# Optimization experiments

Hardware: AMD Instinct MI355X
Metric: run time of the kernel (lower is better)

The kernel has to match this reference:

```python
import jax, jax.numpy as jnp
import numpy as np

B, N, K, D, F, H = 8, 512, 16, 256, 1024, 8


def _ln(x, g, b):
    m = jnp.mean(x, axis=-1, keepdims=True)
    v = jnp.var(x, axis=-1, keepdims=True)
    return (x - m) / jnp.sqrt(v + 1e-5) * g + b


def _mlp(x, W1, b1, W2, b2):
    return jax.nn.gelu(x @ W1 + b1, approximate=False) @ W2 + b2


def setup_inputs() -> dict:
    key = jax.random.key(0)
    ks = jax.random.split(key, 16)
    s = 0.02
    inp = {
        'x': jax.random.normal(ks[0], (N, B, D), jnp.float32),
        'e': jax.random.normal(ks[1], (B, N, K, D), jnp.float32),
        'edge_index': jax.random.randint(ks[2], (B, N, K), 0, N),
        'Wq': jax.random.normal(ks[3], (D, D), jnp.float32) * s,
        'bq': jnp.zeros((D,), jnp.float32),
        'Wk': jax.random.normal(ks[4], (D, D), jnp.float32) * s,
        'bk': jnp.zeros((D,), jnp.float32),
        'Wv': jax.random.normal(ks[5], (D, D), jnp.float32) * s,
        'bv': jnp.zeros((D,), jnp.float32),
        'Wo': jax.random.normal(ks[6], (D, D), jnp.float32) * s,
        'bo': jnp.zeros((D,), jnp.float32),
        'nW1': jax.random.normal(ks[7], (D, F), jnp.float32) * s,
        'nb1': jnp.zeros((F,), jnp.float32),
        'nW2': jax.random.normal(ks[8], (F, D), jnp.float32) * s,
        'nb2': jnp.zeros((D,), jnp.float32),
        'eW1': jax.random.normal(ks[9], (D, F), jnp.float32) * s,
        'eb1': jnp.zeros((F,), jnp.float32),
        'eW2': jax.random.normal(ks[10], (F, D), jnp.float32) * s,
        'eb2': jnp.zeros((D,), jnp.float32),
        'na_g': jnp.ones((D,), jnp.float32), 'na_b': jnp.zeros((D,), jnp.float32),
        'ea_g': jnp.ones((D,), jnp.float32), 'ea_b': jnp.zeros((D,), jnp.float32),
        'nf_g': jnp.ones((D,), jnp.float32), 'nf_b': jnp.zeros((D,), jnp.float32),
        'ef_g': jnp.ones((D,), jnp.float32), 'ef_b': jnp.zeros((D,), jnp.float32),
    }
    return inp


def reference(x, e, edge_index, Wq, bq, Wk, bk, Wv, bv, Wo, bo,
              nW1, nb1, nW2, nb2, eW1, eb1, eW2, eb2,
              na_g, na_b, ea_g, ea_b, nf_g, nf_b, ef_g, ef_b):
    n, b, d = x.shape
    hd = d // H
    xt = jnp.transpose(x, (1, 0, 2))  # (B, N, D) residual in batch-first layout
    bi = jnp.arange(b)[:, None, None]
    ni = jnp.arange(n)[None, :, None]

    # scatter edge features into dense additive attention bias (B, N, N)
    attn_bias = jnp.zeros((b, n, n), x.dtype).at[bi, ni, edge_index].set(e.mean(-1))

    def heads(t):  # (B,N,D) -> (B,H,N,hd)
        return t.reshape(b, n, H, hd).transpose(0, 2, 1, 3)

    q = heads(xt @ Wq + bq) * (hd ** -0.5)
    k = heads(xt @ Wk + bk)
    v = heads(xt @ Wv + bv)
    logits = jnp.einsum('bhnd,bhmd->bhnm', q, k) + attn_bias[:, None]
    attn = jax.nn.softmax(logits, axis=-1)  # (B,H,N,N)
    out = jnp.einsum('bhnm,bhmd->bhnd', attn, v)
    out = out.transpose(0, 2, 1, 3).reshape(b, n, d) @ Wo + bo

    xn = _ln(xt + out, na_g, na_b)  # (B,N,D)

    # edge update: gather attn weights and neighbor node features via edge_index
    weights = attn.mean(axis=1)  # (B,N,N) head-averaged
    w = weights[bi, edge_index, ni]  # (B,N,K): weights[b, edge_index[b,n,k], n]
    gathered = xt[jnp.arange(b)[:, None, None], edge_index]  # (B,N,K,D)
    e2 = _ln(e + w[..., None] * gathered, ea_g, ea_b)

    xn = _ln(xn + _mlp(xn, nW1, nb1, nW2, nb2), nf_g, nf_b)
    e2 = _ln(e2 + _mlp(e2, eW1, eb1, eW2, eb2), ef_g, ef_b)
    return jnp.transpose(xn, (1, 0, 2)), e2
```

## Files before the change

### kernel.cpp

```cpp
#include <hip/hip_runtime.h>
#include <hip/hip_bf16.h>
#include <math.h>

#define B_ 8
#define N_ 512
#define K_ 16
#define D_ 256
#define F_ 1024
#define H_ 8
#define HD_ 32
#define M_ (B_*N_)
#define R_ (B_*N_*K_)

typedef __bf16 bf16x8 __attribute__((ext_vector_type(8)));
typedef float  f32x4  __attribute__((ext_vector_type(4)));

__device__ inline short bf16s(float f) {
    __hip_bfloat16 h = __float2bfloat16(f);
    return *reinterpret_cast<short*>(&h);
}
__device__ inline float b2f(short s) {
    union { float f; unsigned u; } v; v.u = ((unsigned)(unsigned short)s) << 16; return v.f;
}

__device__ __forceinline__ void gload16(const short* g, short* l) {
    __builtin_amdgcn_global_load_lds(
        (const __attribute__((address_space(1))) unsigned int*)g,
        (__attribute__((address_space(3))) unsigned int*)l, 16, 0, 0);
}

__global__ __launch_bounds__(256) void transposeAll(
        const float* __restrict__ Wq, const float* __restrict__ Wk,
        const float* __restrict__ Wv, const float* __restrict__ Wo,
        const float* __restrict__ nW1, const float* __restrict__ nW2,
        const float* __restrict__ eW1, const float* __restrict__ eW2,
        short* __restrict__ WqkvT, short* __restrict__ WoT,
        short* __restrict__ nW1T, short* __restrict__ nW2T,
        short* __restrict__ eW1T, short* __restrict__ eW2T)
{
    const float* W; short* WT; int Kk, Nn; float sc = 1.f;
    switch (blockIdx.z) {
        case 0: W=Wq;  WT=WqkvT;          Kk=256;  Nn=256;  sc=0.17677669529663687f; break;
        case 1: W=Wk;  WT=WqkvT+256*256;  Kk=256;  Nn=256;  break;
        case 2: W=Wv;  WT=WqkvT+512*256;  Kk=256;  Nn=256;  break;
        case 3: W=Wo;  WT=WoT;            Kk=256;  Nn=256;  break;
        case 4: W=nW1; WT=nW1T;           Kk=256;  Nn=1024; break;
        case 5: W=nW2; WT=nW2T;           Kk=1024; Nn=256;  break;
        case 6: W=eW1; WT=eW1T;           Kk=256;  Nn=1024; break;
        default:W=eW2; WT=eW2T;           Kk=1024; Nn=256;  break;
    }
    const int bx = blockIdx.x, by = blockIdx.y;
    if (bx >= Nn/32 || by >= Kk/32) return;
    __shared__ float tile[32][33];
    int tx = threadIdx.x & 31, ty = threadIdx.x >> 5;
    #pragma unroll
    for (int j = 0; j < 4; ++j) {
        int k = by*32 + ty + j*8;
        tile[ty + j*8][tx] = W[(size_t)k*Nn + bx*32 + tx];
    }
    __syncthreads();
    #pragma unroll
    for (int j = 0; j < 4; ++j) {
        int n = bx*32 + ty + j*8;
        WT[(size_t)n*Kk + by*32 + tx] = bf16s(tile[tx][ty + j*8] * sc);
    }
}

__global__ __launch_bounds__(256) void build_bqkv(const float* __restrict__ bq,
        const float* __restrict__ bk, const float* __restrict__ bv,
        float* __restrict__ bqkv)
{
    int t = blockIdx.x*256 + threadIdx.x;
    if (t >= 768) return;
    float v = (t < 256) ? bq[t]*0.17677669529663687f
            : (t < 512) ? bk[t-256] : bv[t-512];
    bqkv[t] = v;
}

__global__ __launch_bounds__(256) void conv_x(const float* __restrict__ x,
        short* __restrict__ xtb)
{
    int row = blockIdx.x;
    int d = threadIdx.x;
    int b = row >> 9, n = row & 511;
    xtb[(size_t)row*D_ + d] = bf16s(x[((size_t)n*B_ + b)*D_ + d]);
}

__global__ __launch_bounds__(256) void edge_means(const float* __restrict__ e,
        float* __restrict__ means)
{
    long row = (long)blockIdx.x*4 + (threadIdx.x >> 6);
    int lane = threadIdx.x & 63;
    float4 v = ((const float4*)(e + row*D_))[lane];
    float s = v.x + v.y + v.z + v.w;
    for (int o = 1; o < 64; o <<= 1) s += __shfl_xor(s, o);
    if (lane == 0) means[row] = s * (1.f/D_);
}

__global__ __launch_bounds__(256) void bias_build(const int* __restrict__ ei,
        const float* __restrict__ means, float* __restrict__ biasb)
{
    const int r0 = blockIdx.x * 16;
    float4* bp4 = (float4*)(biasb + (size_t)r0*N_);
    #pragma unroll
    for (int i = threadIdx.x; i < 16*N_/4; i += 256)
        bp4[i] = make_float4(0.f, 0.f, 0.f, 0.f);
    __syncthreads();
    if (threadIdx.x < 16) {
        const int idx = r0 + threadIdx.x;
        const int* ep = ei + (size_t)idx*K_;
        const float* mp = means + (size_t)idx*K_;
        float* bp = biasb + (size_t)idx*N_;
        for (int k = 0; k < K_; ++k) bp[ep[k]] = mp[k];
    }
}

template<int OUTMODE>
__global__ __launch_bounds__(256) void gemm_bf16(
        const short* __restrict__ A, const short* __restrict__ BT,
        const float* __restrict__ bias, float* __restrict__ Cf,
        short* __restrict__ Cb, short* __restrict__ vtb, int Nn, int Kk)
{
    __shared__ __align__(16) short As[128*32];
    __shared__ __align__(16) short Bs[128*32];
    const int t = threadIdx.x;
    const int lane = t & 63;
    const int wave = t >> 6;
    const int wr = (wave >> 1) * 64;
    const int wc = (wave & 1) * 64;
    const int bm = blockIdx.x, bn = blockIdx.y;
    f32x4 acc[4][4] = {};
    const int srow = lane >> 2;
    const int sk   = (lane & 3) * 8;
    const int fr = lane & 15;
    const int fk = (lane >> 4) * 8;
    for (int k0 = 0; k0 < Kk; k0 += 32) {
        __syncthreads();
        #pragma unroll
        for (int i = 0; i < 2; ++i) {
            const int rb = wave*16 + i*64;
            gload16(A  + (size_t)(bm*128 + rb + srow)*Kk + k0 + sk, &As[rb*32]);
            gload16(BT + (size_t)(bn*128 + rb + srow)*Kk + k0 + sk, &Bs[rb*32]);
        }
        __syncthreads();
        bf16x8 af[4], bfr[4];
        #pragma unroll
        for (int i2 = 0; i2 < 4; ++i2)
            af[i2] = *(const bf16x8*)&As[(wr + i2*16 + fr)*32 + fk];
        #pragma unroll
        for (int n2 = 0; n2 < 4; ++n2)
            bfr[n2] = *(const bf16x8*)&Bs[(wc + n2*16 + fr)*32 + fk];
        #pragma unroll
        for (int i2 = 0; i2 < 4; ++i2)
            #pragma unroll
            for (int n2 = 0; n2 < 4; ++n2)
                acc[i2][n2] = __builtin_amdgcn_mfma_f32_16x16x32_bf16(
                        af[i2], bfr[n2], acc[i2][n2], 0, 0, 0);
    }
    const int fq4 = (lane >> 4) * 4;
    #pragma unroll
    for (int i2 = 0; i2 < 4; ++i2) {
        #pragma unroll
        for (int n2 = 0; n2 < 4; ++n2) {
            const int col = bn*128 + wc + n2*16 + fr;
            const float bv = bias[col];
            if constexpr (OUTMODE == 2) {
                const int rowb = bm*128 + wr + i2*16 + fq4;
                if (col < 512) {
                    #pragma unroll
                    for (int r2 = 0; r2 < 4; ++r2)
                        Cb[(size_t)(rowb + r2)*512 + col] = bf16s(acc[i2][n2][r2] + bv);
                } else {
                    const int b = rowb >> 9, n = rowb & 511;
                    const int dv = col - 512, h = dv >> 5, dh = dv & 31;
                    short4 s4;
                    s4.x = bf16s(acc[i2][n2][0] + bv);
                    s4.y = bf16s(acc[i2][n2][1] + bv);
                    s4.z = bf16s(acc[i2][n2][2] + bv);
                    s4.w = bf16s(acc[i2][n2][3] + bv);
                    *(short4*)&vtb[((size_t)((b*H_ + h)*HD_ + dh))*512 + n] = s4;
                }
            } else {
                #pragma unroll
                for (int r2 = 0; r2 < 4; ++r2) {
                    const int row = bm*128 + wr + i2*16 + fq4 + r2;
                    Cf[(size_t)row*Nn + col] = acc[i2][n2][r2] + bv;
                }
            }
        }
    }
}

__global__ __launch_bounds__(512, 4) void gemm_gelu(
        const short* __restrict__ A, const short* __restrict__ BT,
        const float* __restrict__ bias, short* __restrict__ Cb, int Nn, int Kk)
{
    __shared__ __align__(16) short As[128*32];
    __shared__ __align__(16) short Bs[256*32];
    const int t = threadIdx.x;
    const int lane = t & 63;
    const int wave = t >> 6;
    const int wrg = (wave >> 2) * 64;
    const int wc  = (wave & 3) * 64;
    const int bm = blockIdx.x, bn = blockIdx.y;
    f32x4 acc[4][4] = {};
    const int srow = lane >> 2;
    const int sk   = (lane & 3) * 8;
    const int fr = lane & 15;
    const int fk = (lane >> 4) * 8;
    for (int k0 = 0; k0 < Kk; k0 += 32) {
        __syncthreads();
        {
            const int rb = wave*16;
            gload16(A + (size_t)(bm*128 + rb + srow)*Kk + k0 + sk, &As[rb*32]);
        }
        #pragma unroll
        for (int i = 0; i < 2; ++i) {
            const int rb = wave*16 + i*128;
            gload16(BT + (size_t)(bn*256 + rb + srow)*Kk + k0 + sk, &Bs[rb*32]);
        }
        __syncthreads();
        bf16x8 af[4], bfr[4];
        #pragma unroll
        for (int i2 = 0; i2 < 4; ++i2)
            af[i2] = *(const bf16x8*)&As[(wrg + i2*16 + fr)*32 + fk];
        #pragma unroll
        for (int n2 = 0; n2 < 4; ++n2)
            bfr[n2] = *(const bf16x8*)&Bs[(wc + n2*16 + fr)*32 + fk];
        #pragma unroll
        for (int i2 = 0; i2 < 4; ++i2)
            #pragma unroll
            for (int n2 = 0; n2 < 4; ++n2)
                acc[i2][n2] = __builtin_amdgcn_mfma_f32_16x16x32_bf16(
                        af[i2], bfr[n2], acc[i2][n2], 0, 0, 0);
    }
    const int fq4 = (lane >> 4) * 4;
    #pragma unroll
    for (int i2 = 0; i2 < 4; ++i2) {
        #pragma unroll
        for (int n2 = 0; n2 < 4; ++n2) {
            const int col = bn*256 + wc + n2*16 + fr;
            const float bv = bias[col];
            #pragma unroll
            for (int r2 = 0; r2 < 4; ++r2) {
                const int row = bm*128 + wrg + i2*16 + fq4 + r2;
                float v = acc[i2][n2][r2] + bv;
                v = 0.5f*v*(1.f + erff(v*0.70710678118654752f));
                Cb[(size_t)row*Nn + col] = bf16s(v);
            }
        }
    }
}

template<bool TRANSOUT, bool RESBF>
__global__ __launch_bounds__(512, 4) void gemm_ln2(
        const short* __restrict__ A, const short* __restrict__ BT,
        const float* __restrict__ bias, const float* __restrict__ resf,
        const short* __restrict__ resb,
        const float* __restrict__ g, const float* __restrict__ bt,
        float* __restrict__ out, int Kk)
{
    __shared__ __align__(16) short As[128*32];
    __shared__ __align__(16) short Bs[256*32];
    __shared__ float rs[128][4][2];
    __shared__ float mr[128][2];
    const int t = threadIdx.x;
    const int lane = t & 63;
    const int wave = t >> 6;
    const int wrg = (wave >> 2) * 64;
    const int wc  = (wave & 3) * 64;
    const int bm = blockIdx.x;
    f32x4 acc[4][4] = {};
    const int srow = lane >> 2;
    const int sk   = (lane & 3) * 8;
    const int fr = lane & 15;
    const int fk = (lane >> 4) * 8;
    for (int k0 = 0; k0 < Kk; k0 += 32) {
        __syncthreads();
        {
            const int rb = wave*16;
            gload16(A + (size_t)(bm*128 + rb + srow)*Kk + k0 + sk, &As[rb*32]);
        }
        #pragma unroll
        for (int i = 0; i < 2; ++i) {
            const int rb = wave*16 + i*128;
            gload16(BT + (size_t)(rb + srow)*Kk + k0 + sk, &Bs[rb*32]);
        }
        __syncthreads();
        bf16x8 af[4], bfr[4];
        #pragma unroll
        for (int i2 = 0; i2 < 4; ++i2)
            af[i2] = *(const bf16x8*)&As[(wrg + i2*16 + fr)*32 + fk];
        #pragma unroll
        for (int n2 = 0; n2 < 4; ++n2)
            bfr[n2] = *(const bf16x8*)&Bs[(wc + n2*16 + fr)*32 + fk];
        #pragma unroll
        for (int i2 = 0; i2 < 4; ++i2)
            #pragma unroll
            for (int n2 = 0; n2 < 4; ++n2)
                acc[i2][n2] = __builtin_amdgcn_mfma_f32_16x16x32_bf16(
                        af[i2], bfr[n2], acc[i2][n2], 0, 0, 0);
    }
    const int fq4 = (lane >> 4) * 4;
    float ps[4][4] = {}, pq[4][4] = {};
    #pragma unroll
    for (int i2 = 0; i2 < 4; ++i2) {
        #pragma unroll
        for (int n2 = 0; n2 < 4; ++n2) {
            const int c = wc + n2*16 + fr;
            const float bv = bias[c];
            #pragma unroll
            for (int r2 = 0; r2 < 4; ++r2) {
                const int row = wrg + i2*16 + fq4 + r2;
                const size_t grow = (size_t)bm*128 + row;
                float rv;
                if constexpr (RESBF) rv = b2f(resb[grow*256 + c]);
                else                 rv = resf[grow*256 + c];
                float v = acc[i2][n2][r2] + bv + rv;
                acc[i2][n2][r2] = v;
                ps[i2][r2] += v;
                pq[i2][r2] += v*v;
            }
        }
    }
    #pragma unroll
    for (int i2 = 0; i2 < 4; ++i2)
        #pragma unroll
        for (int r2 = 0; r2 < 4; ++r2)
            #pragma unroll
            for (int o = 1; o < 16; o <<= 1) {
                ps[i2][r2] += __shfl_xor(ps[i2][r2], o);
                pq[i2][r2] += __shfl_xor(pq[i2][r2], o);
            }
    if ((lane & 15) == 0) {
        #pragma unroll
        for (int i2 = 0; i2 < 4; ++i2)
            #pragma unroll
            for (int r2 = 0; r2 < 4; ++r2) {
                const int row = wrg + i2*16 + fq4 + r2;
                rs[row][wave & 3][0] = ps[i2][r2];
                rs[row][wave & 3][1] = pq[i2][r2];
            }
    }
    __syncthreads();
    if (t < 128) {
        float S = 0.f, Q = 0.f;
        #pragma unroll
        for (int w = 0; w < 4; ++w) { S += rs[t][w][0]; Q += rs[t][w][1]; }
        const float mean = S * (1.f/D_);
        mr[t][0] = mean;
        mr[t][1] = rsqrtf(Q * (1.f/D_) - mean*mean + 1e-5f);
    }
    __syncthreads();
    #pragma unroll
    for (int i2 = 0; i2 < 4; ++i2) {
        #pragma unroll
        for (int n2 = 0; n2 < 4; ++n2) {
            const int c = wc + n2*16 + fr;
            const float gv = g[c], bv2 = bt[c];
            #pragma unroll
            for (int r2 = 0; r2 < 4; ++r2) {
                const int row = wrg + i2*16 + fq4 + r2;
                const size_t grow = (size_t)bm*128 + row;
                const float o = (acc[i2][n2][r2] - mr[row][0])*mr[row][1]*gv + bv2;
                if constexpr (TRANSOUT) {
                    const int bb = (int)(grow >> 9), nn = (int)(grow & 511);
                    out[((size_t)nn*B_ + bb)*D_ + c] = o;
                } else {
                    out[grow*256 + c] = o;
                }
            }
        }
    }
}

__global__ __launch_bounds__(256) void attn_fused(const short* __restrict__ qkb,
        const short* __restrict__ vtb, const float* __restrict__ biasb,
        float* __restrict__ rowsum, short* __restrict__ actx)
{
    __shared__ __align__(16) short Qs[128*32];
    __shared__ __align__(16) short Ks[128*32];
    __shared__ __align__(16) short Vs[32*128];
    __shared__ __align__(16) short Ps[128*128];
    const int it = blockIdx.x, bh = blockIdx.y;
    const int b = bh >> 3, h = bh & 7;
    const int t = threadIdx.x;
    const int lane = t & 63;
    const int wave = t >> 6;
    const int wr0 = wave * 32;
    const int srow = lane >> 2;
    const int sk   = (lane & 3) * 8;
    const int srow8 = lane >> 4;
    const int ck16  = lane & 15;
    const int fr = lane & 15;
    const int fk = (lane >> 4) * 8;
    const int fq4 = (lane >> 4) * 4;
    const int I0 = it * 128;
    #pragma unroll
    for (int i = 0; i < 2; ++i) {
        const int rb = wave*16 + i*64;
        gload16(qkb + (size_t)(b*N_ + I0 + rb + srow)*512 + h*HD_ + sk, &Qs[rb*32]);
    }
    float rsum[2][4] = {};
    f32x4 apv[2][2] = {};
    const float LOG2E = 1.4426950408889634f;
    for (int jt = 0; jt < 4; ++jt) {
        const int J0 = jt * 128;
        __syncthreads();
        #pragma unroll
        for (int i = 0; i < 2; ++i) {
            const int rb = wave*16 + i*64;
            gload16(qkb + (size_t)(b*N_ + J0 + rb + srow)*512 + 256 + h*HD_ + sk, &Ks[rb*32]);
        }
        #pragma unroll
        for (int i = 0; i < 2; ++i) {
            const int db = wave*8 + i*4;
            const int dh = db + srow8;
            gload16(vtb + ((size_t)bh*HD_ + dh)*512 + J0 + ((ck16 ^ (dh & 7)) * 8),
                    &Vs[db*128]);
        }
        __syncthreads();
        bf16x8 aq[2], kf8[8];
        #pragma unroll
        for (int i2 = 0; i2 < 2; ++i2)
            aq[i2] = *(const bf16x8*)&Qs[(wr0 + i2*16 + fr)*32 + fk];
        #pragma unroll
        for (int n2 = 0; n2 < 8; ++n2)
            kf8[n2] = *(const bf16x8*)&Ks[(n2*16 + fr)*32 + fk];
        #pragma unroll
        for (int i2 = 0; i2 < 2; ++i2) {
            #pragma unroll
            for (int n2 = 0; n2 < 8; ++n2) {
                f32x4 z = {0.f, 0.f, 0.f, 0.f};
                f32x4 s = __builtin_amdgcn_mfma_f32_16x16x32_bf16(aq[i2], kf8[n2], z, 0, 0, 0);
                const int jg = J0 + n2*16 + fr;
                #pragma unroll
                for (int r2 = 0; r2 < 4; ++r2) {
                    const int rloc = wr0 + i2*16 + fq4 + r2;
                    const float l = s[r2] + biasb[((size_t)b*N_ + I0 + rloc)*N_ + jg];
                    const float p = exp2f(fminf(l, 80.f) * LOG2E);
                    rsum[i2][r2] += p;
                    int idx = rloc*128 + n2*16 + fr;
                    idx ^= (rloc & 7) << 3;
                    Ps[idx] = bf16s(p);
                }
            }
        }
        __syncthreads();
        #pragma unroll
        for (int ks = 0; ks < 4; ++ks) {
            bf16x8 ap[2], bv[2];
            #pragma unroll
            for (int i2 = 0; i2 < 2; ++i2) {
                const int r = wr0 + i2*16 + fr;
                int idx = r*128 + ks*32 + fk;
                idx ^= (r & 7) << 3;
                ap[i2] = *(const bf16x8*)&Ps[idx];
            }
            #pragma unroll
            for (int n2 = 0; n2 < 2; ++n2) {
                const int dh = n2*16 + fr;
                const int q = lane >> 4;
                const int slot = (ks*4 + q) ^ (dh & 7);
                bv[n2] = *(const bf16x8*)&Vs[dh*128 + slot*8];
            }
            #pragma unroll
            for (int i2 = 0; i2 < 2; ++i2)
                #pragma unroll
                for (int n2 = 0; n2 < 2; ++n2)
                    apv[i2][n2] = __builtin_amdgcn_mfma_f32_16x16x32_bf16(
                            ap[i2], bv[n2], apv[i2][n2], 0, 0, 0);
        }
    }
    #pragma unroll
    for (int i2 = 0; i2 < 2; ++i2)
        #pragma unroll
        for (int r2 = 0; r2 < 4; ++r2)
            #pragma unroll
            for (int o = 1; o < 16; o <<= 1)
                rsum[i2][r2] += __shfl_xor(rsum[i2][r2], o);
    #pragma unroll
    for (int i2 = 0; i2 < 2; ++i2) {
        #pragma unroll
        for (int r2 = 0; r2 < 4; ++r2) {
            const int row = wr0 + i2*16 + fq4 + r2;
            if (fr == 0)
                rowsum[(size_t)bh*N_ + I0 + row] = rsum[i2][r2];
            const float inv = 1.f / rsum[i2][r2];
            #pragma unroll
            for (int n2 = 0; n2 < 2; ++n2)
                actx[((size_t)b*N_ + I0 + row)*D_ + h*HD_ + n2*16 + fr]
                    = bf16s(apv[i2][n2][r2] * inv);
        }
    }
}

__device__ inline void ln_core(float v[4], int lane, const float* __restrict__ g,
        const float* __restrict__ bt, float out[4])
{
    float s  = v[0] + v[1] + v[2] + v[3];
    float sq = v[0]*v[0] + v[1]*v[1] + v[2]*v[2] + v[3]*v[3];
    for (int o = 1; o < 64; o <<= 1) { s += __shfl_xor(s, o); sq += __shfl_xor(sq, o); }
    float mean = s * (1.f/D_);
    float rstd = rsqrtf(sq * (1.f/D_) - mean*mean + 1e-5f);
    const float4 gv = *(const float4*)(g  + lane*4);
    const float4 bv = *(const float4*)(bt + lane*4);
    out[0] = (v[0]-mean)*rstd*gv.x + bv.x;
    out[1] = (v[1]-mean)*rstd*gv.y + bv.y;
    out[2] = (v[2]-mean)*rstd*gv.z + bv.z;
    out[3] = (v[3]-mean)*rstd*gv.w + bv.w;
}

__global__ __launch_bounds__(256) void ln_xn(const float* __restrict__ x,
        const float* __restrict__ aout, const float* __restrict__ g,
        const float* __restrict__ bt, float* __restrict__ xn, short* __restrict__ xnb)
{
    int row = blockIdx.x*4 + (threadIdx.x >> 6);
    int lane = threadIdx.x & 63;
    int b = row >> 9, n = row & 511;
    const float4 xv = *(const float4*)(x + ((size_t)n*B_ + b)*D_ + lane*4);
    const float4 av = *(const float4*)(aout + (size_t)row*D_ + lane*4);
    float v[4] = {xv.x+av.x, xv.y+av.y, xv.z+av.z, xv.w+av.w};
    float o[4];
    ln_core(v, lane, g, bt, o);
    *(float4*)(xn + (size_t)row*D_ + lane*4) = make_float4(o[0], o[1], o[2], o[3]);
    short4 s4; s4.x = bf16s(o[0]); s4.y = bf16s(o[1]); s4.z = bf16s(o[2]); s4.w = bf16s(o[3]);
    *(short4*)(xnb + (size_t)row*D_ + lane*4) = s4;
}

__global__ __launch_bounds__(256) void edge_update(const float* __restrict__ e,
        const float* __restrict__ x, const int* __restrict__ ei,
        const short* __restrict__ qkb, const float* __restrict__ biasb,
        const float* __restrict__ rowsum, const float* __restrict__ g,
        const float* __restrict__ bt, short* __restrict__ e2b)
{
    long row = (long)blockIdx.x*4 + (threadIdx.x >> 6);
    int lane = threadIdx.x & 63;
    long bi = row >> 4;
    long b = bi / N_; int i = (int)(bi % N_);
    int ej = ei[row];
    const short4 q4 = *(const short4*)(qkb + ((size_t)b*N_ + ej)*512 + lane*4);
    const short4 k4 = *(const short4*)(qkb + ((size_t)b*N_ + i)*512 + 256 + lane*4);
    float dot = b2f(q4.x)*b2f(k4.x) + b2f(q4.y)*b2f(k4.y)
              + b2f(q4.z)*b2f(k4.z) + b2f(q4.w)*b2f(k4.w);
    dot += __shfl_xor(dot, 1); dot += __shfl_xor(dot, 2); dot += __shfl_xor(dot, 4);
    const int h = lane >> 3;
    const float l = dot + biasb[((size_t)b*N_ + ej)*N_ + i];
    float p = exp2f(fminf(l, 80.f) * 1.4426950408889634f)
            / rowsum[((size_t)b*H_ + h)*N_ + ej];
    p += __shfl_xor(p, 8); p += __shfl_xor(p, 16); p += __shfl_xor(p, 32);
    const float w = p * (1.f/H_);
    const float4 ev = *(const float4*)(e + row*D_ + lane*4);
    const float4 xv = *(const float4*)(x + ((size_t)ej*B_ + b)*D_ + lane*4);
    float v[4] = {ev.x + w*xv.x, ev.y + w*xv.y, ev.z + w*xv.z, ev.w + w*xv.w};
    float o[4];
    ln_core(v, lane, g, bt, o);
    short4 s4; s4.x = bf16s(o[0]); s4.y = bf16s(o[1]); s4.z = bf16s(o[2]); s4.w = bf16s(o[3]);
    *(short4*)(e2b + row*D_ + lane*4) = s4;
}

extern "C" void kernel_launch(void* const* d_in, const int* in_sizes, int n_in,
                              void* d_out, int out_size, void* d_ws, size_t ws_size,
                              hipStream_t stream)
{
    (void)in_sizes; (void)n_in; (void)out_size; (void)ws_size;
    const float* x    = (const float*)d_in[0];
    const float* e    = (const float*)d_in[1];
    const int*   ei   = (const int*)d_in[2];
    const float* Wq   = (const float*)d_in[3];
    const float* bq   = (const float*)d_in[4];
    const float* Wk   = (const float*)d_in[5];
    const float* bk   = (const float*)d_in[6];
    const float* Wv   = (const float*)d_in[7];
    const float* bv   = (const float*)d_in[8];
    const float* Wo   = (const float*)d_in[9];
    const float* bo   = (const float*)d_in[10];
    const float* nW1  = (const float*)d_in[11];
    const float* nb1  = (const float*)d_in[12];
    const float* nW2  = (const float*)d_in[13];
    const float* nb2  = (const float*)d_in[14];
    const float* eW1  = (const float*)d_in[15];
    const float* eb1  = (const float*)d_in[16];
    const float* eW2  = (const float*)d_in[17];
    const float* eb2  = (const float*)d_in[18];
    const float* na_g = (const float*)d_in[19];
    const float* na_b = (const float*)d_in[20];
    const float* ea_g = (const float*)d_in[21];
    const float* ea_b = (const float*)d_in[22];
    const float* nf_g = (const float*)d_in[23];
    const float* nf_b = (const float*)d_in[24];
    const float* ef_g = (const float*)d_in[25];
    const float* ef_b = (const float*)d_in[26];

    float* out1 = (float*)d_out;
    float* e2f  = out1 + (size_t)N_*B_*D_;

    char* wp = (char*)d_ws;
    auto alloc = [&](size_t bytes) -> char* {
        char* p = wp; wp += (bytes + 255) & ~(size_t)255; return p;
    };
    short* WqkvT  = (short*)alloc((size_t)768*D_*2);
    float* bqkv   = (float*)alloc(768*4);
    short* WoT    = (short*)alloc((size_t)D_*D_*2);
    short* nW1T   = (short*)alloc((size_t)F_*D_*2);
    short* nW2T   = (short*)alloc((size_t)D_*F_*2);
    short* eW1T   = (short*)alloc((size_t)F_*D_*2);
    short* eW2T   = (short*)alloc((size_t)D_*F_*2);
    float* rowsum = (float*)alloc((size_t)B_*H_*N_*4);
    short* e2b    = (short*)alloc((size_t)R_*D_*2);
    char* ov = wp;
    auto allocA = [&](size_t bytes) -> char* {
        char* p = ov; ov += (bytes + 255) & ~(size_t)255; return p;
    };
    short* xtb    = (short*)allocA((size_t)M_*D_*2);
    float* means  = (float*)allocA((size_t)R_*4);
    float* biasb  = (float*)allocA((size_t)B_*N_*N_*4);
    short* qkb    = (short*)allocA((size_t)M_*512*2);
    short* vtb    = (short*)allocA((size_t)B_*H_*HD_*N_*2);
    short* actx   = (short*)allocA((size_t)M_*D_*2);
    float* aout   = (float*)allocA((size_t)M_*D_*4);
    float* xn     = (float*)allocA((size_t)M_*D_*4);
    short* xnb    = (short*)allocA((size_t)M_*D_*2);
    short* nhid   = (short*)allocA((size_t)M_*F_*2);
    short* ehid   = (short*)wp;

    transposeAll<<<dim3(32, 32, 8), 256, 0, stream>>>(Wq, Wk, Wv, Wo,
            nW1, nW2, eW1, eW2, WqkvT, WoT, nW1T, nW2T, eW1T, eW2T);
    build_bqkv<<<3, 256, 0, stream>>>(bq, bk, bv, bqkv);
    conv_x<<<M_, 256, 0, stream>>>(x, xtb);

    edge_means<<<R_/4, 256, 0, stream>>>(e, means);
    bias_build<<<M_/16, 256, 0, stream>>>(ei, means, biasb);

    gemm_bf16<2><<<dim3(M_/128, 768/128), 256, 0, stream>>>(
            xtb, WqkvT, bqkv, nullptr, qkb, vtb, 768, D_);

    attn_fused<<<dim3(N_/128, B_*H_), 256, 0, stream>>>(qkb, vtb, biasb, rowsum, actx);
    gemm_bf16<0><<<dim3(M_/128, D_/128), 256, 0, stream>>>(
            actx, WoT, bo, aout, nullptr, nullptr, D_, D_);

    ln_xn<<<M_/4, 256, 0, stream>>>(x, aout, na_g, na_b, xn, xnb);
    gemm_gelu<<<dim3(M_/128, F_/256), 512, 0, stream>>>(
            xnb, nW1T, nb1, nhid, F_, D_);
    gemm_ln2<true,false><<<M_/128, 512, 0, stream>>>(
            nhid, nW2T, nb2, xn, nullptr, nf_g, nf_b, out1, F_);

    edge_update<<<R_/4, 256, 0, stream>>>(e, x, ei, qkb, biasb, rowsum,
            ea_g, ea_b, e2b);
    gemm_gelu<<<dim3(R_/128, F_/256), 512, 0, stream>>>(
            e2b, eW1T, eb1, ehid, F_, D_);
    gemm_ln2<false,true><<<R_/128, 512, 0, stream>>>(
            ehid, eW2T, eb2, nullptr, e2b, ef_g, ef_b, e2f, F_);
}
```

Measured before the change: 331.8 us.

## Fuse Wo projection with residual LayerNorm and chunk edge MLP for cache reuse

```diff
diff --git a/kernel.cpp b/kernel.cpp
--- a/kernel.cpp
+++ b/kernel.cpp
@@ -11,6 +11,8 @@
 #define HD_ 32
 #define M_ (B_*N_)
 #define R_ (B_*N_*K_)
+#define RC_ 16384
+#define NCH_ (R_/RC_)
 
 typedef __bf16 bf16x8 __attribute__((ext_vector_type(8)));
 typedef float  f32x4  __attribute__((ext_vector_type(4)));
@@ -115,11 +117,10 @@
     }
 }
 
-template<int OUTMODE>
-__global__ __launch_bounds__(256) void gemm_bf16(
+__global__ __launch_bounds__(256) void gemm_qkv(
         const short* __restrict__ A, const short* __restrict__ BT,
-        const float* __restrict__ bias, float* __restrict__ Cf,
-        short* __restrict__ Cb, short* __restrict__ vtb, int Nn, int Kk)
+        const float* __restrict__ bias, short* __restrict__ Cb,
+        short* __restrict__ vtb, int Kk)
 {
     __shared__ __align__(16) short As[128*32];
     __shared__ __align__(16) short Bs[128*32];
@@ -164,28 +165,20 @@
         for (int n2 = 0; n2 < 4; ++n2) {
             const int col = bn*128 + wc + n2*16 + fr;
             const float bv = bias[col];
-            if constexpr (OUTMODE == 2) {
-                const int rowb = bm*128 + wr + i2*16 + fq4;
-                if (col < 512) {
-                    #pragma unroll
-                    for (int r2 = 0; r2 < 4; ++r2)
-                        Cb[(size_t)(rowb + r2)*512 + col] = bf16s(acc[i2][n2][r2] + bv);
-                } else {
-                    const int b = rowb >> 9, n = rowb & 511;
-                    const int dv = col - 512, h = dv >> 5, dh = dv & 31;
-                    short4 s4;
-                    s4.x = bf16s(acc[i2][n2][0] + bv);
-                    s4.y = bf16s(acc[i2][n2][1] + bv);
-                    s4.z = bf16s(acc[i2][n2][2] + bv);
-                    s4.w = bf16s(acc[i2][n2][3] + bv);
-                    *(short4*)&vtb[((size_t)((b*H_ + h)*HD_ + dh))*512 + n] = s4;
-                }
+            const int rowb = bm*128 + wr + i2*16 + fq4;
+            if (col < 512) {
+                #pragma unroll
+                for (int r2 = 0; r2 < 4; ++r2)
+                    Cb[(size_t)(rowb + r2)*512 + col] = bf16s(acc[i2][n2][r2] + bv);
             } else {
-                #pragma unroll
-                for (int r2 = 0; r2 < 4; ++r2) {
-                    const int row = bm*128 + wr + i2*16 + fq4 + r2;
-                    Cf[(size_t)row*Nn + col] = acc[i2][n2][r2] + bv;
-                }
+                const int b = rowb >> 9, n = rowb & 511;
+                const int dv = col - 512, h = dv >> 5, dh = dv & 31;
+                short4 s4;
+                s4.x = bf16s(acc[i2][n2][0] + bv);
+                s4.y = bf16s(acc[i2][n2][1] + bv);
+                s4.z = bf16s(acc[i2][n2][2] + bv);
+                s4.w = bf16s(acc[i2][n2][3] + bv);
+                *(short4*)&vtb[((size_t)((b*H_ + h)*HD_ + dh))*512 + n] = s4;
             }
         }
     }
@@ -252,13 +245,13 @@
     }
 }
 
-template<bool TRANSOUT, bool RESBF>
+template<bool TRANSOUT, int RESMODE, bool DUALOUT>
 __global__ __launch_bounds__(512, 4) void gemm_ln2(
         const short* __restrict__ A, const short* __restrict__ BT,
         const float* __restrict__ bias, const float* __restrict__ resf,
         const short* __restrict__ resb,
         const float* __restrict__ g, const float* __restrict__ bt,
-        float* __restrict__ out, int Kk)
+        float* __restrict__ out, short* __restrict__ outb, int Kk)
 {
     __shared__ __align__(16) short As[128*32];
     __shared__ __align__(16) short Bs[256*32];
@@ -314,8 +307,11 @@
                 const int row = wrg + i2*16 + fq4 + r2;
                 const size_t grow = (size_t)bm*128 + row;
                 float rv;
-                if constexpr (RESBF) rv = b2f(resb[grow*256 + c]);
-                else                 rv = resf[grow*256 + c];
+                if constexpr (RESMODE == 1) rv = b2f(resb[grow*256 + c]);
+                else if constexpr (RESMODE == 2) {
+                    const int bb = (int)(grow >> 9), nn = (int)(grow & 511);
+                    rv = resf[((size_t)nn*B_ + bb)*256 + c];
+                } else rv = resf[grow*256 + c];
                 float v = acc[i2][n2][r2] + bv + rv;
                 acc[i2][n2][r2] = v;
                 ps[i2][r2] += v;
@@ -369,6 +365,8 @@
                 } else {
                     out[grow*256 + c] = o;
                 }
+                if constexpr (DUALOUT)
+                    outb[grow*256 + c] = bf16s(o);
             }
         }
     }
@@ -509,23 +507,6 @@
     out[1] = (v[1]-mean)*rstd*gv.y + bv.y;
     out[2] = (v[2]-mean)*rstd*gv.z + bv.z;
     out[3] = (v[3]-mean)*rstd*gv.w + bv.w;
-}
-
-__global__ __launch_bounds__(256) void ln_xn(const float* __restrict__ x,
-        const float* __restrict__ aout, const float* __restrict__ g,
-        const float* __restrict__ bt, float* __restrict__ xn, short* __restrict__ xnb)
-{
-    int row = blockIdx.x*4 + (threadIdx.x >> 6);
-    int lane = threadIdx.x & 63;
-    int b = row >> 9, n = row & 511;
-    const float4 xv = *(const float4*)(x + ((size_t)n*B_ + b)*D_ + lane*4);
-    const float4 av = *(const float4*)(aout + (size_t)row*D_ + lane*4);
-    float v[4] = {xv.x+av.x, xv.y+av.y, xv.z+av.z, xv.w+av.w};
-    float o[4];
-    ln_core(v, lane, g, bt, o);
-    *(float4*)(xn + (size_t)row*D_ + lane*4) = make_float4(o[0], o[1], o[2], o[3]);
-    short4 s4; s4.x = bf16s(o[0]); s4.y = bf16s(o[1]); s4.z = bf16s(o[2]); s4.w = bf16s(o[3]);
-    *(short4*)(xnb + (size_t)row*D_ + lane*4) = s4;
 }
 
 __global__ __launch_bounds__(256) void edge_update(const float* __restrict__ e,
@@ -618,7 +599,6 @@
     short* qkb    = (short*)allocA((size_t)M_*512*2);
     short* vtb    = (short*)allocA((size_t)B_*H_*HD_*N_*2);
     short* actx   = (short*)allocA((size_t)M_*D_*2);
-    float* aout   = (float*)allocA((size_t)M_*D_*4);
     float* xn     = (float*)allocA((size_t)M_*D_*4);
     short* xnb    = (short*)allocA((size_t)M_*D_*2);
     short* nhid   = (short*)allocA((size_t)M_*F_*2);
@@ -632,23 +612,27 @@
     edge_means<<<R_/4, 256, 0, stream>>>(e, means);
     bias_build<<<M_/16, 256, 0, stream>>>(ei, means, biasb);
 
-    gemm_bf16<2><<<dim3(M_/128, 768/128), 256, 0, stream>>>(
-            xtb, WqkvT, bqkv, nullptr, qkb, vtb, 768, D_);
+    gemm_qkv<<<dim3(M_/128, 768/128), 256, 0, stream>>>(
+            xtb, WqkvT, bqkv, qkb, vtb, D_);
 
     attn_fused<<<dim3(N_/128, B_*H_), 256, 0, stream>>>(qkb, vtb, biasb, rowsum, actx);
-    gemm_bf16<0><<<dim3(M_/128, D_/128), 256, 0, stream>>>(
-            actx, WoT, bo, aout, nullptr, nullptr, D_, D_);
-
-    ln_xn<<<M_/4, 256, 0, stream>>>(x, aout, na_g, na_b, xn, xnb);
+
+    gemm_ln2<false,2,true><<<M_/128, 512, 0, stream>>>(
+            actx, WoT, bo, x, nullptr, na_g, na_b, xn, xnb, D_);
+
     gemm_gelu<<<dim3(M_/128, F_/256), 512, 0, stream>>>(
             xnb, nW1T, nb1, nhid, F_, D_);
-    gemm_ln2<true,false><<<M_/128, 512, 0, stream>>>(
-            nhid, nW2T, nb2, xn, nullptr, nf_g, nf_b, out1, F_);
+    gemm_ln2<true,0,false><<<M_/128, 512, 0, stream>>>(
+            nhid, nW2T, nb2, xn, nullptr, nf_g, nf_b, out1, nullptr, F_);
 
     edge_update<<<R_/4, 256, 0, stream>>>(e, x, ei, qkb, biasb, rowsum,
             ea_g, ea_b, e2b);
-    gemm_gelu<<<dim3(R_/128, F_/256), 512, 0, stream>>>(
-            e2b, eW1T, eb1, ehid, F_, D_);
-    gemm_ln2<false,true><<<R_/128, 512, 0, stream>>>(
-            ehid, eW2T, eb2, nullptr, e2b, ef_g, ef_b, e2f, F_);
-}
+    for (int c = 0; c < NCH_; ++c) {
+        const size_t off = (size_t)c*RC_*D_;
+        gemm_gelu<<<dim3(RC_/128, F_/256), 512, 0, stream>>>(
+                e2b + off, eW1T, eb1, ehid, F_, D_);
+        gemm_ln2<false,1,false><<<RC_/128, 512, 0, stream>>>(
+                ehid, eW2T, eb2, nullptr, e2b + off, ef_g, ef_b,
+                e2f + off, nullptr, F_);
+    }
+}
```

New measurement: 462.5 us. 39.4% more time.
